# Kernel optimization log

Measured on AMD Instinct MI355X. Metric: run time of the kernel, lower is better.

Reference implementation:

```python
import jax, jax.numpy as jnp
import numpy as np

N = 131072      # total nodes across batched graphs
E = 524288      # total directed edges (avg degree 4, molecular graphs)
F_NODE = 64     # raw atom features
F_BOND = 16     # raw bond features
D = 128         # hidden width (hard-coded in the module)
H2 = 16
G = 4096        # number of graphs in the batch
DIM_OUT = 1


def _make_params(key):
    ks = iter(jax.random.split(key, 64))
    def w(shape, scale):
        return jax.random.normal(next(ks), shape, jnp.float32) * scale
    p = {"fc1_w": w((F_NODE, D), 0.1), "fc1_b": jnp.zeros((D,), jnp.float32)}
    for l in (1, 2, 3):
        p[f"gc{l}_wq"] = w((D, D), 0.05); p[f"gc{l}_bq"] = jnp.zeros((D,), jnp.float32)
        p[f"gc{l}_wk"] = w((D, D), 0.05); p[f"gc{l}_bk"] = jnp.zeros((D,), jnp.float32)
        p[f"gc{l}_wv"] = w((D, D), 0.05); p[f"gc{l}_bv"] = jnp.zeros((D,), jnp.float32)
        p[f"gc{l}_we"] = w((F_BOND, D), 0.05)   # PyG lin_edge has no bias
        p[f"gc{l}_ws"] = w((D, D), 0.05); p[f"gc{l}_bs"] = jnp.zeros((D,), jnp.float32)
    p["fc2_w"] = w((D, H2), 0.1); p["fc2_b"] = jnp.zeros((H2,), jnp.float32)
    p["fc3_w"] = w((H2, DIM_OUT), 0.1); p["fc3_b"] = jnp.zeros((DIM_OUT,), jnp.float32)
    return p


def setup_inputs() -> dict:
    key = jax.random.key(0)
    k1, k2, k3, k4, kp = jax.random.split(key, 5)
    inp = {
        "x": jax.random.normal(k1, (N, F_NODE), jnp.float32),
        "edge_index": jax.random.randint(k2, (2, E), 0, N),
        "edge_attr": jax.random.normal(k3, (E, F_BOND), jnp.float32),
        "batch": jnp.sort(jax.random.randint(k4, (N,), 0, G)),
    }
    inp.update(_make_params(kp))
    return inp


def _tconv(x, src, dst, edge_attr, wq, bq, wk, bk, wv, bv, we, ws, bs):
    # PyG TransformerConv, heads=1, concat=True, beta=False, root_weight=True
    n = x.shape[0]
    q = x @ wq + bq                                   # [N,D]
    k = x @ wk + bk                                   # [N,D]
    v = x @ wv + bv                                   # [N,D]
    e = edge_attr @ we                                # [E,D] edge projection
    kj = k[src] + e                                   # key_j + edge
    vj = v[src] + e                                   # value_j + edge
    alpha = jnp.sum(q[dst] * kj, axis=-1) / jnp.sqrt(jnp.float32(D))   # [E]
    # segment softmax over incoming edges of each dst node
    amax = jax.ops.segment_max(alpha, dst, num_segments=n)
    ex = jnp.exp(alpha - amax[dst])
    denom = jax.ops.segment_sum(ex, dst, num_segments=n)
    w = ex / denom[dst]                               # [E]
    agg = jax.ops.segment_sum(vj * w[:, None], dst, num_segments=n)    # scatter-add
    return agg + x @ ws + bs                          # skip / root weight


def reference(x, edge_index, edge_attr, batch,
              fc1_w, fc1_b,
              gc1_wq, gc1_bq, gc1_wk, gc1_bk, gc1_wv, gc1_bv, gc1_we, gc1_ws, gc1_bs,
              gc2_wq, gc2_bq, gc2_wk, gc2_bk, gc2_wv, gc2_bv, gc2_we, gc2_ws, gc2_bs,
              gc3_wq, gc3_bq, gc3_wk, gc3_bk, gc3_wv, gc3_bv, gc3_we, gc3_ws, gc3_bs,
              fc2_w, fc2_b, fc3_w, fc3_b):
    src, dst = edge_index[0], edge_index[1]
    h = x @ fc1_w + fc1_b
    layers = [
        (gc1_wq, gc1_bq, gc1_wk, gc1_bk, gc1_wv, gc1_bv, gc1_we, gc1_ws, gc1_bs),
        (gc2_wq, gc2_bq, gc2_wk, gc2_bk, gc2_wv, gc2_bv, gc2_we, gc2_ws, gc2_bs),
        (gc3_wq, gc3_bq, gc3_wk, gc3_bk, gc3_wv, gc3_bv, gc3_we, gc3_ws, gc3_bs),
    ]
    for p in layers:
        h = jax.nn.relu(_tconv(h, src, dst, edge_attr, *p))
    # global mean pool over graph ids
    cnt = jax.ops.segment_sum(jnp.ones((h.shape[0],), h.dtype), batch, num_segments=G)
    hg = jax.ops.segment_sum(h, batch, num_segments=G) / jnp.maximum(cnt, 1.0)[:, None]
    h = jax.nn.relu(hg @ fc2_w + fc2_b)
    return h @ fc3_w + fc3_b                          # [G, DIM_OUT]
```

## Files before the change

kernel.cpp:

```cpp
#include <hip/hip_runtime.h>
#include <hip/hip_fp16.h>


#define D 128

typedef _Float16 half8 __attribute__((ext_vector_type(8)));
typedef float f32x4 __attribute__((ext_vector_type(4)));

__global__ __launch_bounds__(256) void hist_kernel(const int* __restrict__ dst,
                                                   int* __restrict__ counts, int e) {
  int i = blockIdx.x * 256 + threadIdx.x;
  if (i < e) atomicAdd(&counts[dst[i]], 1);
}

__global__ __launch_bounds__(256) void scan_a_kernel(const int* __restrict__ counts,
                                                     int* __restrict__ incl,
                                                     int* __restrict__ bsum) {
  int gid = blockIdx.x * 256 + threadIdx.x;
  int lane = threadIdx.x & 63, wid = threadIdx.x >> 6;
  int v = counts[gid];
  int s = v;
  #pragma unroll
  for (int off = 1; off < 64; off <<= 1) {
    int t = __shfl_up(s, off, 64);
    if (lane >= off) s += t;
  }
  __shared__ int wsum[4];
  if (lane == 63) wsum[wid] = s;
  __syncthreads();
  #pragma unroll
  for (int w = 0; w < 3; ++w)
    if (wid > w) s += wsum[w];
  incl[gid] = s;
  if (threadIdx.x == 255) bsum[blockIdx.x] = s;
}

__global__ __launch_bounds__(512) void scan_b_kernel(int* __restrict__ bs) {
  int tid = threadIdx.x;
  int lane = tid & 63, wid = tid >> 6;
  int v = bs[tid];
  int s = v;
  #pragma unroll
  for (int off = 1; off < 64; off <<= 1) {
    int t = __shfl_up(s, off, 64);
    if (lane >= off) s += t;
  }
  __shared__ int wsum[8];
  if (lane == 63) wsum[wid] = s;
  __syncthreads();
  #pragma unroll
  for (int w = 0; w < 7; ++w)
    if (wid > w) s += wsum[w];
  bs[tid] = s - v;
}

__global__ __launch_bounds__(256) void scan_c_kernel(const int* __restrict__ incl,
                                                     const int* __restrict__ counts,
                                                     const int* __restrict__ bsum,
                                                     int* __restrict__ offs, int n, int e) {
  int gid = blockIdx.x * 256 + threadIdx.x;
  if (gid < n) offs[gid] = incl[gid] - counts[gid] + bsum[blockIdx.x];
  if (gid == 0) offs[n] = e;
}

__global__ __launch_bounds__(256) void scatter_kernel(const int* __restrict__ srcs,
                                                      const int* __restrict__ dsts,
                                                      const int* __restrict__ offs,
                                                      int* __restrict__ cursor,
                                                      int* __restrict__ csr_src,
                                                      int* __restrict__ csr_eid, int e) {
  int i = blockIdx.x * 256 + threadIdx.x;
  if (i >= e) return;
  int d = dsts[i];
  int slot = atomicAdd(&cursor[d], 1);
  int p = offs[d] + slot;
  csr_src[p] = srcs[i];
  csr_eid[p] = i;
}

__global__ __launch_bounds__(256) void sort_kernel(const int* __restrict__ offs,
                                                   int* __restrict__ eid,
                                                   int* __restrict__ srcs, int n) {
  int i = blockIdx.x * 256 + threadIdx.x;
  if (i >= n) return;
  int b = offs[i], e = offs[i + 1];
  for (int p = b + 1; p < e; ++p) {
    int ke = eid[p], ks = srcs[p];
    int q = p - 1;
    while (q >= b && eid[q] > ke) {
      eid[q + 1] = eid[q]; srcs[q + 1] = srcs[q]; --q;
    }
    eid[q + 1] = ke; srcs[q + 1] = ks;
  }
}

__global__ __launch_bounds__(256) void convw_kernel(const float* __restrict__ W,
                                                    __half* __restrict__ out,
                                                    int ncols, int K) {
  int idx = blockIdx.x * 256 + threadIdx.x;
  if (idx >= ncols * K) return;
  int n = idx / K, kk = idx - n * K;
  out[idx] = __float2half(W[(size_t)kk * ncols + n]);
}

__global__ __launch_bounds__(256) void convwe_kernel(const float* __restrict__ we,
                                                     const float* __restrict__ Wq,
                                                     const float* __restrict__ bq,
                                                     __half* __restrict__ outW,
                                                     float* __restrict__ outB) {
  int idx = blockIdx.x * 256 + threadIdx.x;
  if (idx < 2048) {
    int f = idx >> 7, kk = idx & 127;
    float s = 0.f;
    for (int d = 0; d < 128; ++d) s += we[f * 128 + d] * Wq[kk * 128 + d];
    outW[f * 128 + kk] = __float2half(s);
  } else if (idx < 2064) {
    int f = idx - 2048;
    float s = 0.f;
    for (int d = 0; d < 128; ++d) s += we[f * 128 + d] * bq[d];
    outB[f] = s;
  }
}

__global__ __launch_bounds__(256) void bcat_kernel(const float* __restrict__ bq,
                                                   const float* __restrict__ bk,
                                                   const float* __restrict__ bv,
                                                   const float* __restrict__ bs,
                                                   float* __restrict__ out) {
  int j = blockIdx.x * 256 + threadIdx.x;
  if (j >= 512) return;
  const float* src = (j < 128) ? bq : (j < 256) ? bk : (j < 384) ? bv : bs;
  out[j] = src[j & 127];
}

__device__ inline void store4h(__half* p, float4 v) {
  __half2 h01 = __floats2half2_rn(v.x, v.y);
  __half2 h23 = __floats2half2_rn(v.z, v.w);
  uint2 u;
  u.x = *(unsigned int*)&h01;
  u.y = *(unsigned int*)&h23;
  *(uint2*)p = u;
}

__device__ inline void load8h(const __half* p, float4& lo, float4& hi) {
  uint4 u = *(const uint4*)p;
  float2 a = __half22float2(*(__half2*)&u.x);
  float2 b = __half22float2(*(__half2*)&u.y);
  float2 c = __half22float2(*(__half2*)&u.z);
  float2 d = __half22float2(*(__half2*)&u.w);
  lo = make_float4(a.x, a.y, b.x, b.y);
  hi = make_float4(c.x, c.y, d.x, d.y);
}

template <int K, int NCT, bool QKVS>
__global__ __launch_bounds__(256) void mfma_gemm_kernel(
    const float* in, const __half* __restrict__ Wt, const float* __restrict__ bias,
    __half* __restrict__ qkv, float* os, float* __restrict__ qt) {
  constexpr int WST = K + 8;
  __shared__ alignas(16) __half Wc[128 * WST];
  const int tid = threadIdx.x;
  const int w = tid >> 6, l = tid & 63;
  const int lo = l & 15, hi = l >> 4;
  const size_t row = (size_t)blockIdx.x * 64 + w * 16 + lo;

  half8 af[K / 32];
  #pragma unroll
  for (int s = 0; s < K / 32; ++s) {
    const float* sp = in + row * K + s * 32 + hi * 8;
    float4 f0 = *(const float4*)sp;
    float4 f1 = *(const float4*)(sp + 4);
    half8 a;
    a[0] = (_Float16)f0.x; a[1] = (_Float16)f0.y; a[2] = (_Float16)f0.z; a[3] = (_Float16)f0.w;
    a[4] = (_Float16)f1.x; a[5] = (_Float16)f1.y; a[6] = (_Float16)f1.z; a[7] = (_Float16)f1.w;
    af[s] = a;
  }

  #pragma unroll 1
  for (int ch = 0; ch < NCT / 8; ++ch) {
    __syncthreads();
    #pragma unroll
    for (int i = 0; i < 128 * K / 8 / 256; ++i) {
      int idx = i * 256 + tid;
      int col = idx / (K / 8), kk = (idx % (K / 8)) * 8;
      *(uint4*)&Wc[col * WST + kk] =
          *(const uint4*)(Wt + (size_t)(ch * 128 + col) * K + kk);
    }
    __syncthreads();

    #pragma unroll
    for (int t = 0; t < 8; ++t) {
      f32x4 c = {0.f, 0.f, 0.f, 0.f};
      #pragma unroll
      for (int s = 0; s < K / 32; ++s) {
        half8 bf = *(const half8*)&Wc[(t * 16 + lo) * WST + s * 32 + hi * 8];
        c = __builtin_amdgcn_mfma_f32_16x16x32_f16(bf, af[s], c, 0, 0, 0);
      }
      const int col0 = ch * 128 + t * 16 + hi * 4;
      float4 b4 = *(const float4*)(bias + col0);
      float4 o;
      o.x = c[0] + b4.x; o.y = c[1] + b4.y; o.z = c[2] + b4.z; o.w = c[3] + b4.w;
      if (QKVS) {
        const int mid = col0 >> 7, cc = col0 & 127;
        if (mid < 3) store4h(qkv + row * 384 + mid * 128 + cc, o);
        else         *(float4*)(os + row * 128 + cc) = o;
      } else {
        *(float4*)(os + row * 128 + col0) = o;
      }
    }
  }

  if constexpr (QKVS) {
    __syncthreads();
    {
      int col = tid >> 4;
      int kk = (tid & 15) * 8;
      *(uint4*)&Wc[col * WST + kk] =
          *(const uint4*)(Wt + (size_t)(512 + col) * K + kk);
    }
    __syncthreads();
    f32x4 c = {0.f, 0.f, 0.f, 0.f};
    #pragma unroll
    for (int s = 0; s < K / 32; ++s) {
      half8 bf = *(const half8*)&Wc[lo * WST + s * 32 + hi * 8];
      c = __builtin_amdgcn_mfma_f32_16x16x32_f16(bf, af[s], c, 0, 0, 0);
    }
    float4 b4 = *(const float4*)(bias + 512 + hi * 4);
    float4 o;
    o.x = c[0] + b4.x; o.y = c[1] + b4.y; o.z = c[2] + b4.z; o.w = c[3] + b4.w;
    *(float4*)(qt + row * 16 + hi * 4) = o;
  }
}

__global__ __launch_bounds__(256) void node_kernel(
    const __half* __restrict__ qkv, float* __restrict__ h,
    const float* __restrict__ edge_attr,
    const float* __restrict__ we, const float* __restrict__ tq,
    const int* __restrict__ offs, const int* __restrict__ csr_src,
    const int* __restrict__ csr_eid) {
  __shared__ float we_s[16 * 160];
  for (int i = threadIdx.x; i < 2048; i += 256) {
    int f = i >> 7, d = i & 127;
    we_s[f * 160 + (d >> 3) * 10 + (d & 7)] = we[i];
  }
  __syncthreads();

  const int lane = threadIdx.x & 63;
  const int wid = threadIdx.x >> 6;
  const int g = lane >> 4, sub = lane & 15;
  const int nid = blockIdx.x * 16 + wid * 4 + g;
  const int d0 = sub * 8;
  const float inv_sqrt_d = 0.08838834764831845f;

  float4 qlo, qhi;
  load8h(qkv + (size_t)nid * 384 + d0, qlo, qhi);
  float4 slo = *(const float4*)(h + (size_t)nid * D + d0);
  float4 shi = *(const float4*)(h + (size_t)nid * D + d0 + 4);
  const float tf = tq[(size_t)nid * 16 + sub];

  const int eb = offs[nid], ee = offs[nid + 1];
  float m = -3.0e38f, den = 0.f, accE = 0.f;
  float4 alo = {0.f, 0.f, 0.f, 0.f}, ahi = {0.f, 0.f, 0.f, 0.f};

  float4 klon = {0,0,0,0}, khin = {0,0,0,0}, vlon = {0,0,0,0}, vhin = {0,0,0,0};
  float eafn = 0.f;
  int p = eb;
  if (p < ee) {
    int src = csr_src[p];
    int eid = csr_eid[p];
    load8h(qkv + (size_t)src * 384 + 128 + d0, klon, khin);
    load8h(qkv + (size_t)src * 384 + 256 + d0, vlon, vhin);
    eafn = edge_attr[(size_t)eid * 16 + sub];
  }
  while (p < ee) {
    float4 klo = klon, khi = khin, vlo = vlon, vhi = vhin;
    float eaf = eafn;
    ++p;
    if (p < ee) {
      int src = csr_src[p];
      int eid = csr_eid[p];
      load8h(qkv + (size_t)src * 384 + 128 + d0, klon, khin);
      load8h(qkv + (size_t)src * 384 + 256 + d0, vlon, vhin);
      eafn = edge_attr[(size_t)eid * 16 + sub];
    }
    float pa = qlo.x * klo.x + qlo.y * klo.y + qlo.z * klo.z + qlo.w * klo.w +
               qhi.x * khi.x + qhi.y * khi.y + qhi.z * khi.z + qhi.w * khi.w +
               eaf * tf;
    #pragma unroll
    for (int off = 8; off > 0; off >>= 1) pa += __shfl_xor(pa, off, 64);
    pa *= inv_sqrt_d;
    float mn = fmaxf(m, pa);
    float esc = __expf(m - mn);
    float ew = __expf(pa - mn);
    den = den * esc + ew;
    alo.x = alo.x * esc + ew * vlo.x;
    alo.y = alo.y * esc + ew * vlo.y;
    alo.z = alo.z * esc + ew * vlo.z;
    alo.w = alo.w * esc + ew * vlo.w;
    ahi.x = ahi.x * esc + ew * vhi.x;
    ahi.y = ahi.y * esc + ew * vhi.y;
    ahi.z = ahi.z * esc + ew * vhi.z;
    ahi.w = ahi.w * esc + ew * vhi.w;
    accE = accE * esc + ew * eaf;
    m = mn;
  }

  if (den > 0.f) {
    float inv = 1.0f / den;
    float4 elo = {0.f, 0.f, 0.f, 0.f}, ehi = {0.f, 0.f, 0.f, 0.f};
    const int gbase = lane & 48;
    const int wb = sub * 10;
    #pragma unroll
    for (int f = 0; f < 16; ++f) {
      float aE = __shfl(accE, gbase + f, 64);
      const float* wr = &we_s[f * 160 + wb];
      float2 w01 = *(const float2*)(wr + 0);
      float2 w23 = *(const float2*)(wr + 2);
      float2 w45 = *(const float2*)(wr + 4);
      float2 w67 = *(const float2*)(wr + 6);
      elo.x += aE * w01.x; elo.y += aE * w01.y; elo.z += aE * w23.x; elo.w += aE * w23.y;
      ehi.x += aE * w45.x; ehi.y += aE * w45.y; ehi.z += aE * w67.x; ehi.w += aE * w67.y;
    }
    slo.x += (alo.x + elo.x) * inv;
    slo.y += (alo.y + elo.y) * inv;
    slo.z += (alo.z + elo.z) * inv;
    slo.w += (alo.w + elo.w) * inv;
    shi.x += (ahi.x + ehi.x) * inv;
    shi.y += (ahi.y + ehi.y) * inv;
    shi.z += (ahi.z + ehi.z) * inv;
    shi.w += (ahi.w + ehi.w) * inv;
  }
  slo.x = fmaxf(slo.x, 0.f); slo.y = fmaxf(slo.y, 0.f);
  slo.z = fmaxf(slo.z, 0.f); slo.w = fmaxf(slo.w, 0.f);
  shi.x = fmaxf(shi.x, 0.f); shi.y = fmaxf(shi.y, 0.f);
  shi.z = fmaxf(shi.z, 0.f); shi.w = fmaxf(shi.w, 0.f);
  *(float4*)(h + (size_t)nid * D + d0) = slo;
  *(float4*)(h + (size_t)nid * D + d0 + 4) = shi;
}

__global__ __launch_bounds__(64) void pool_kernel(const float* __restrict__ h,
                                                  const int* __restrict__ batch,
                                                  float* __restrict__ hg,
                                                  float* __restrict__ cnt, int n) {
  int base = blockIdx.x * 128;
  int lane = threadIdx.x;
  float2 acc = {0.f, 0.f};
  float run = 0.f;
  int cur = batch[base];
  for (int i = 0; i < 128; ++i) {
    int node = base + i;
    int g = batch[node];
    if (g != cur) {
      atomicAdd(&hg[(size_t)cur * D + 2 * lane], acc.x);
      atomicAdd(&hg[(size_t)cur * D + 2 * lane + 1], acc.y);
      if (lane == 0) atomicAdd(&cnt[cur], run);
      acc.x = acc.y = 0.f; run = 0.f; cur = g;
    }
    float2 hv = *(const float2*)(h + (size_t)node * D + 2 * lane);
    acc.x += hv.x; acc.y += hv.y; run += 1.f;
  }
  atomicAdd(&hg[(size_t)cur * D + 2 * lane], acc.x);
  atomicAdd(&hg[(size_t)cur * D + 2 * lane + 1], acc.y);
  if (lane == 0) atomicAdd(&cnt[cur], run);
}

__global__ __launch_bounds__(256) void head_kernel(const float* __restrict__ hg,
                                                   const float* __restrict__ cnt,
                                                   const float* __restrict__ w2,
                                                   const float* __restrict__ b2,
                                                   const float* __restrict__ w3,
                                                   const float* __restrict__ b3,
                                                   float* __restrict__ out) {
  __shared__ float w2s[128 * 16];
  __shared__ float rowb[4][128];
  for (int i = threadIdx.x; i < (128 * 16) / 4; i += 256)
    ((float4*)w2s)[i] = ((const float4*)w2)[i];
  int wid = threadIdx.x >> 6, lane = threadIdx.x & 63;
  int g = blockIdx.x * 4 + wid;
  float inv = 1.0f / fmaxf(cnt[g], 1.0f);
  rowb[wid][lane] = hg[(size_t)g * D + lane] * inv;
  rowb[wid][lane + 64] = hg[(size_t)g * D + 64 + lane] * inv;
  __syncthreads();
  float t = 0.f;
  if (lane < 16) {
    float a = b2[lane];
    for (int d = 0; d < 128; ++d) a += rowb[wid][d] * w2s[d * 16 + lane];
    t = fmaxf(a, 0.f) * w3[lane];
  }
  #pragma unroll
  for (int off = 8; off > 0; off >>= 1) t += __shfl_xor(t, off, 64);
  if (lane == 0) out[g] = t + b3[0];
}

extern "C" void kernel_launch(void* const* d_in, const int* in_sizes, int n_in,
                              void* d_out, int out_size, void* d_ws, size_t ws_size,
                              hipStream_t stream) {
  const float* x = (const float*)d_in[0];
  const int* eidx = (const int*)d_in[1];
  const float* eattr = (const float*)d_in[2];
  const int* batch = (const int*)d_in[3];
  const float* fc1_w = (const float*)d_in[4];
  const float* fc1_b = (const float*)d_in[5];
  const float* WQ[3] = {(const float*)d_in[6], (const float*)d_in[15], (const float*)d_in[24]};
  const float* BQ[3] = {(const float*)d_in[7], (const float*)d_in[16], (const float*)d_in[25]};
  const float* WK[3] = {(const float*)d_in[8], (const float*)d_in[17], (const float*)d_in[26]};
  const float* BK[3] = {(const float*)d_in[9], (const float*)d_in[18], (const float*)d_in[27]};
  const float* WV[3] = {(const float*)d_in[10], (const float*)d_in[19], (const float*)d_in[28]};
  const float* BV[3] = {(const float*)d_in[11], (const float*)d_in[20], (const float*)d_in[29]};
  const float* WE[3] = {(const float*)d_in[12], (const float*)d_in[21], (const float*)d_in[30]};
  const float* WS[3] = {(const float*)d_in[13], (const float*)d_in[22], (const float*)d_in[31]};
  const float* BS[3] = {(const float*)d_in[14], (const float*)d_in[23], (const float*)d_in[32]};
  const float* fc2_w = (const float*)d_in[33];
  const float* fc2_b = (const float*)d_in[34];
  const float* fc3_w = (const float*)d_in[35];
  const float* fc3_b = (const float*)d_in[36];

  const int N = in_sizes[0] / 64;
  const int E = in_sizes[1] / 2;
  const int G = out_size;
  const int* srcs = eidx;
  const int* dsts = eidx + E;
  const size_t ND = (size_t)N * D;

  char* base = (char*)d_ws;
  size_t off = 0;
  auto alloc = [&](size_t bytes) {
    void* p = base + off;
    off = (off + bytes + 255) & ~(size_t)255;
    return p;
  };
  float* hg = (float*)alloc((size_t)G * D * 4);
  float* cntf = (float*)alloc((size_t)G * 4);
  int* counts = (int*)alloc((size_t)N * 4);
  int* cursor = (int*)alloc((size_t)N * 4);
  size_t zero_bytes = off;
  int* incl = (int*)alloc((size_t)N * 4);
  int* offs = (int*)alloc((size_t)(N + 4) * 4);
  int* bsum = (int*)alloc(512 * 4);
  int* csr_src = (int*)alloc((size_t)E * 4);
  int* csr_eid = (int*)alloc((size_t)E * 4);
  float* h = (float*)alloc(ND * 4);
  __half* qkv = (__half*)alloc((size_t)N * 384 * 2);
  float* qt = (float*)alloc((size_t)N * 16 * 4);
  __half* Wt[3];
  float* bc[3];
  for (int l = 0; l < 3; ++l) {
    Wt[l] = (__half*)alloc(528 * 128 * 2);
    bc[l] = (float*)alloc(544 * 4);
  }
  __half* fc1t = (__half*)alloc(128 * 64 * 2);
  if (off > ws_size) return;

  hipMemsetAsync(hg, 0, zero_bytes, stream);

  for (int l = 0; l < 3; ++l) {
    convw_kernel<<<64, 256, 0, stream>>>(WQ[l], Wt[l] + 0 * 16384, 128, 128);
    convw_kernel<<<64, 256, 0, stream>>>(WK[l], Wt[l] + 1 * 16384, 128, 128);
    convw_kernel<<<64, 256, 0, stream>>>(WV[l], Wt[l] + 2 * 16384, 128, 128);
    convw_kernel<<<64, 256, 0, stream>>>(WS[l], Wt[l] + 3 * 16384, 128, 128);
    convwe_kernel<<<9, 256, 0, stream>>>(WE[l], WQ[l], BQ[l],
                                         Wt[l] + 4 * 16384, bc[l] + 512);
    bcat_kernel<<<2, 256, 0, stream>>>(BQ[l], BK[l], BV[l], BS[l], bc[l]);
  }
  convw_kernel<<<32, 256, 0, stream>>>(fc1_w, fc1t, 128, 64);

  hist_kernel<<<E / 256, 256, 0, stream>>>(dsts, counts, E);
  scan_a_kernel<<<N / 256, 256, 0, stream>>>(counts, incl, bsum);
  scan_b_kernel<<<1, 512, 0, stream>>>(bsum);
  scan_c_kernel<<<N / 256, 256, 0, stream>>>(incl, counts, bsum, offs, N, E);
  scatter_kernel<<<E / 256, 256, 0, stream>>>(srcs, dsts, offs, cursor, csr_src, csr_eid, E);
  sort_kernel<<<N / 256, 256, 0, stream>>>(offs, csr_eid, csr_src, N);

  mfma_gemm_kernel<64, 8, false><<<N / 64, 256, 0, stream>>>(
      x, fc1t, fc1_b, nullptr, h, nullptr);

  for (int l = 0; l < 3; ++l) {
    mfma_gemm_kernel<128, 32, true><<<N / 64, 256, 0, stream>>>(
        h, Wt[l], bc[l], qkv, h, qt);
    node_kernel<<<N / 16, 256, 0, stream>>>(qkv, h, eattr, WE[l], qt,
                                            offs, csr_src, csr_eid);
  }

  pool_kernel<<<N / 128, 64, 0, stream>>>(h, batch, hg, cntf, N);
  head_kernel<<<G / 4, 256, 0, stream>>>(hg, cntf, fc2_w, fc2_b, fc3_w, fc3_b, (float*)d_out);
}
```

Baseline: 632.3 us.

## Split interleaved QKV buffer into separate arrays and merge weight-prep launches

```diff
diff --git a/kernel.cpp b/kernel.cpp
--- a/kernel.cpp
+++ b/kernel.cpp
@@ -94,43 +94,53 @@
   }
 }
 
-__global__ __launch_bounds__(256) void convw_kernel(const float* __restrict__ W,
-                                                    __half* __restrict__ out,
-                                                    int ncols, int K) {
-  int idx = blockIdx.x * 256 + threadIdx.x;
-  if (idx >= ncols * K) return;
-  int n = idx / K, kk = idx - n * K;
-  out[idx] = __float2half(W[(size_t)kk * ncols + n]);
-}
-
-__global__ __launch_bounds__(256) void convwe_kernel(const float* __restrict__ we,
-                                                     const float* __restrict__ Wq,
-                                                     const float* __restrict__ bq,
-                                                     __half* __restrict__ outW,
-                                                     float* __restrict__ outB) {
-  int idx = blockIdx.x * 256 + threadIdx.x;
-  if (idx < 2048) {
-    int f = idx >> 7, kk = idx & 127;
-    float s = 0.f;
-    for (int d = 0; d < 128; ++d) s += we[f * 128 + d] * Wq[kk * 128 + d];
-    outW[f * 128 + kk] = __float2half(s);
-  } else if (idx < 2064) {
-    int f = idx - 2048;
-    float s = 0.f;
-    for (int d = 0; d < 128; ++d) s += we[f * 128 + d] * bq[d];
-    outB[f] = s;
-  }
-}
-
-__global__ __launch_bounds__(256) void bcat_kernel(const float* __restrict__ bq,
-                                                   const float* __restrict__ bk,
-                                                   const float* __restrict__ bv,
-                                                   const float* __restrict__ bs,
-                                                   float* __restrict__ out) {
-  int j = blockIdx.x * 256 + threadIdx.x;
-  if (j >= 512) return;
-  const float* src = (j < 128) ? bq : (j < 256) ? bk : (j < 384) ? bv : bs;
-  out[j] = src[j & 127];
+struct PrepArgs {
+  const float* W[12];
+  const float* WE[3];
+  const float* BQ[3];
+  const float* BK[3];
+  const float* BV[3];
+  const float* BS[3];
+  const float* fc1w;
+  __half* Wt[3];
+  float* bc[3];
+  __half* fc1t;
+};
+
+__global__ __launch_bounds__(256) void prep_kernel(PrepArgs a) {
+  int b = blockIdx.x, tid = threadIdx.x;
+  if (b < 768) {
+    int m = b >> 6;
+    int l = m >> 2, s = m & 3;
+    int idx = ((b & 63) << 8) | tid;
+    int n = idx >> 7, kk = idx & 127;
+    a.Wt[l][s * 16384 + idx] = __float2half(a.W[m][(size_t)kk * 128 + n]);
+  } else if (b < 800) {
+    int idx = ((b - 768) << 8) | tid;
+    int n = idx >> 6, kk = idx & 63;
+    a.fc1t[idx] = __float2half(a.fc1w[(size_t)kk * 128 + n]);
+  } else if (b < 827) {
+    int l = (b - 800) / 9;
+    int idx = ((b - 800) % 9) * 256 + tid;
+    if (idx < 2048) {
+      int f = idx >> 7, kk = idx & 127;
+      float s = 0.f;
+      for (int d = 0; d < 128; ++d)
+        s += a.WE[l][f * 128 + d] * a.W[l * 4][(size_t)kk * 128 + d];
+      a.Wt[l][4 * 16384 + f * 128 + kk] = __float2half(s);
+    } else if (idx < 2064) {
+      int f = idx - 2048;
+      float s = 0.f;
+      for (int d = 0; d < 128; ++d) s += a.WE[l][f * 128 + d] * a.BQ[l][d];
+      a.bc[l][512 + f] = s;
+    }
+  } else {
+    int l = (b - 827) >> 1;
+    int j = ((b - 827) & 1) * 256 + tid;
+    const float* src = (j < 128) ? a.BQ[l] : (j < 256) ? a.BK[l]
+                     : (j < 384) ? a.BV[l] : a.BS[l];
+    a.bc[l][j] = src[j & 127];
+  }
 }
 
 __device__ inline void store4h(__half* p, float4 v) {
@@ -155,7 +165,8 @@
 template <int K, int NCT, bool QKVS>
 __global__ __launch_bounds__(256) void mfma_gemm_kernel(
     const float* in, const __half* __restrict__ Wt, const float* __restrict__ bias,
-    __half* __restrict__ qkv, float* os, float* __restrict__ qt) {
+    __half* __restrict__ oq, __half* __restrict__ ok, __half* __restrict__ ov,
+    float* os, float* __restrict__ qt) {
   constexpr int WST = K + 8;
   __shared__ alignas(16) __half Wc[128 * WST];
   const int tid = threadIdx.x;
@@ -201,8 +212,10 @@
       o.x = c[0] + b4.x; o.y = c[1] + b4.y; o.z = c[2] + b4.z; o.w = c[3] + b4.w;
       if (QKVS) {
         const int mid = col0 >> 7, cc = col0 & 127;
-        if (mid < 3) store4h(qkv + row * 384 + mid * 128 + cc, o);
-        else         *(float4*)(os + row * 128 + cc) = o;
+        if (mid == 0)      store4h(oq + row * 128 + cc, o);
+        else if (mid == 1) store4h(ok + row * 128 + cc, o);
+        else if (mid == 2) store4h(ov + row * 128 + cc, o);
+        else               *(float4*)(os + row * 128 + cc) = o;
       } else {
         *(float4*)(os + row * 128 + col0) = o;
       }
@@ -232,8 +245,8 @@
 }
 
 __global__ __launch_bounds__(256) void node_kernel(
-    const __half* __restrict__ qkv, float* __restrict__ h,
-    const float* __restrict__ edge_attr,
+    const __half* __restrict__ q, const __half* __restrict__ k, const __half* __restrict__ v,
+    float* __restrict__ h, const float* __restrict__ edge_attr,
     const float* __restrict__ we, const float* __restrict__ tq,
     const int* __restrict__ offs, const int* __restrict__ csr_src,
     const int* __restrict__ csr_eid) {
@@ -252,7 +265,7 @@
   const float inv_sqrt_d = 0.08838834764831845f;
 
   float4 qlo, qhi;
-  load8h(qkv + (size_t)nid * 384 + d0, qlo, qhi);
+  load8h(q + (size_t)nid * D + d0, qlo, qhi);
   float4 slo = *(const float4*)(h + (size_t)nid * D + d0);
   float4 shi = *(const float4*)(h + (size_t)nid * D + d0 + 4);
   const float tf = tq[(size_t)nid * 16 + sub];
@@ -267,8 +280,8 @@
   if (p < ee) {
     int src = csr_src[p];
     int eid = csr_eid[p];
-    load8h(qkv + (size_t)src * 384 + 128 + d0, klon, khin);
-    load8h(qkv + (size_t)src * 384 + 256 + d0, vlon, vhin);
+    load8h(k + (size_t)src * D + d0, klon, khin);
+    load8h(v + (size_t)src * D + d0, vlon, vhin);
     eafn = edge_attr[(size_t)eid * 16 + sub];
   }
   while (p < ee) {
@@ -278,8 +291,8 @@
     if (p < ee) {
       int src = csr_src[p];
       int eid = csr_eid[p];
-      load8h(qkv + (size_t)src * 384 + 128 + d0, klon, khin);
-      load8h(qkv + (size_t)src * 384 + 256 + d0, vlon, vhin);
+      load8h(k + (size_t)src * D + d0, klon, khin);
+      load8h(v + (size_t)src * D + d0, vlon, vhin);
       eafn = edge_attr[(size_t)eid * 16 + sub];
     }
     float pa = qlo.x * klo.x + qlo.y * klo.y + qlo.z * klo.z + qlo.w * klo.w +
@@ -439,7 +452,9 @@
   int* csr_src = (int*)alloc((size_t)E * 4);
   int* csr_eid = (int*)alloc((size_t)E * 4);
   float* h = (float*)alloc(ND * 4);
-  __half* qkv = (__half*)alloc((size_t)N * 384 * 2);
+  __half* q = (__half*)alloc(ND * 2);
+  __half* k = (__half*)alloc(ND * 2);
+  __half* v = (__half*)alloc(ND * 2);
   float* qt = (float*)alloc((size_t)N * 16 * 4);
   __half* Wt[3];
   float* bc[3];
@@ -452,16 +467,19 @@
 
   hipMemsetAsync(hg, 0, zero_bytes, stream);
 
+  PrepArgs pa;
   for (int l = 0; l < 3; ++l) {
-    convw_kernel<<<64, 256, 0, stream>>>(WQ[l], Wt[l] + 0 * 16384, 128, 128);
-    convw_kernel<<<64, 256, 0, stream>>>(WK[l], Wt[l] + 1 * 16384, 128, 128);
-    convw_kernel<<<64, 256, 0, stream>>>(WV[l], Wt[l] + 2 * 16384, 128, 128);
-    convw_kernel<<<64, 256, 0, stream>>>(WS[l], Wt[l] + 3 * 16384, 128, 128);
-    convwe_kernel<<<9, 256, 0, stream>>>(WE[l], WQ[l], BQ[l],
-                                         Wt[l] + 4 * 16384, bc[l] + 512);
-    bcat_kernel<<<2, 256, 0, stream>>>(BQ[l], BK[l], BV[l], BS[l], bc[l]);
-  }
-  convw_kernel<<<32, 256, 0, stream>>>(fc1_w, fc1t, 128, 64);
+    pa.W[l * 4 + 0] = WQ[l];
+    pa.W[l * 4 + 1] = WK[l];
+    pa.W[l * 4 + 2] = WV[l];
+    pa.W[l * 4 + 3] = WS[l];
+    pa.WE[l] = WE[l];
+    pa.BQ[l] = BQ[l]; pa.BK[l] = BK[l]; pa.BV[l] = BV[l]; pa.BS[l] = BS[l];
+    pa.Wt[l] = Wt[l]; pa.bc[l] = bc[l];
+  }
+  pa.fc1w = fc1_w;
+  pa.fc1t = fc1t;
+  prep_kernel<<<833, 256, 0, stream>>>(pa);
 
   hist_kernel<<<E / 256, 256, 0, stream>>>(dsts, counts, E);
   scan_a_kernel<<<N / 256, 256, 0, stream>>>(counts, incl, bsum);
@@ -471,12 +489,12 @@
   sort_kernel<<<N / 256, 256, 0, stream>>>(offs, csr_eid, csr_src, N);
 
   mfma_gemm_kernel<64, 8, false><<<N / 64, 256, 0, stream>>>(
-      x, fc1t, fc1_b, nullptr, h, nullptr);
+      x, fc1t, fc1_b, nullptr, nullptr, nullptr, h, nullptr);
 
   for (int l = 0; l < 3; ++l) {
     mfma_gemm_kernel<128, 32, true><<<N / 64, 256, 0, stream>>>(
-        h, Wt[l], bc[l], qkv, h, qt);
-    node_kernel<<<N / 16, 256, 0, stream>>>(qkv, h, eattr, WE[l], qt,
+        h, Wt[l], bc[l], q, k, v, h, qt);
+    node_kernel<<<N / 16, 256, 0, stream>>>(q, k, v, h, eattr, WE[l], qt,
                                             offs, csr_src, csr_eid);
   }
 
```

Result: faster. 598.4 us (-5.4%).
